# Kernel optimization log

Hardware: AMD Instinct MI355X
Metric: run time of the kernel (lower is better)

The kernel has to match this reference:

```python
import jax, jax.numpy as jnp
import numpy as np

IMG_SIZE = 640.0
CONF_THRESH = 0.001
NMS_THRESH = 0.6
TOP_K = 1000  # fixed-shape candidate cap per class


def _pairwise_iou(b):
    # b: [K,4] in x1,y1,x2,y2; replicates the numpy NMS math (1e-28 / 1e-14 eps)
    x1, y1, x2, y2 = b[:, 0], b[:, 1], b[:, 2], b[:, 3]
    areas = (x2 - x1) * (y2 - y1)
    xx1 = jnp.maximum(x1[:, None], x1[None, :])
    yy1 = jnp.maximum(y1[:, None], y1[None, :])
    xx2 = jnp.minimum(x2[:, None], x2[None, :])
    yy2 = jnp.minimum(y2[:, None], y2[None, :])
    w = jnp.maximum(1e-28, xx2 - xx1)
    h = jnp.maximum(1e-28, yy2 - yy1)
    inter = w * h
    return inter / (areas[:, None] + areas[None, :] - inter + 1e-14)


def setup_inputs() -> dict:
    key = jax.random.key(0)
    k1, k2, k3 = jax.random.split(key, 3)
    img_size, strides, KA, C = 640, [8, 16, 32], 3, 80
    anchor = np.array([[10, 13], [16, 30], [33, 23], [30, 61], [62, 45], [59, 119],
                       [116, 90], [156, 198], [373, 326]], np.float32).reshape(3, 3, 2)
    grids, anchs, strs = [], [], []
    for lvl, s in enumerate(strides):
        f = img_size // s
        gy, gx = np.meshgrid(np.arange(f), np.arange(f), indexing='ij')
        gxy = np.stack([gx, gy], -1).reshape(-1, 1, 2).astype(np.float32)
        grids.append(np.broadcast_to(gxy, (f * f, KA, 2)).reshape(-1, 2))
        anchs.append(np.broadcast_to(anchor[lvl][None], (f * f, KA, 2)).reshape(-1, 2).astype(np.float32))
        strs.append(np.full((f * f * KA, 1), s, np.float32))
    grid_xy = jnp.asarray(np.concatenate(grids, 0))      # [N,2]
    anchors_wh = jnp.asarray(np.concatenate(anchs, 0))   # [N,2]
    stride_t = jnp.asarray(np.concatenate(strs, 0))      # [N,1]
    N = grid_xy.shape[0]  # 25200
    return {
        'reg_pred': jax.random.normal(k1, (N, 4), jnp.float32),
        'obj_pred': jax.random.normal(k2, (N, 1), jnp.float32),
        'cls_pred': jax.random.normal(k3, (N, C), jnp.float32),
        'grid_xy': grid_xy,
        'anchors_wh': anchors_wh,
        'stride_t': stride_t,
    }


def reference(reg_pred, obj_pred, cls_pred, grid_xy, anchors_wh, stride_t):
    # ---- box decode (YOLO head) ----
    xy = (jax.nn.sigmoid(reg_pred[:, :2]) + grid_xy) * stride_t       # centers in pixels
    wh = jnp.exp(reg_pred[:, 2:]) * anchors_wh                        # sizes in pixels
    boxes = jnp.concatenate([xy - 0.5 * wh, xy + 0.5 * wh], axis=-1)  # [N,4]
    boxes = jnp.clip(boxes / IMG_SIZE, 0.0, 1.0)
    # ---- scoring: sigmoid(obj) * softmax(cls) ----
    scores_all = jax.nn.sigmoid(obj_pred) * jax.nn.softmax(cls_pred, axis=-1)  # [N,C]
    cls_inds = jnp.argmax(scores_all, axis=-1)          # [N]
    scores = jnp.max(scores_all, axis=-1)               # [N]
    C = cls_pred.shape[-1]
    K = TOP_K
    ar = jnp.arange(K)

    def nms_class(c):
        s_c = jnp.where((cls_inds == c) & (scores >= CONF_THRESH), scores, -1.0)
        vals, idx = jax.lax.top_k(s_c, K)               # sorted desc, fixed shape
        b = boxes[idx]                                  # [K,4]
        valid = vals > 0.0
        iou = _pairwise_iou(b)                          # [K,K]

        def body(i, keep):
            sup = keep[i] & (iou[i] > NMS_THRESH) & (ar > i)
            return keep & ~sup

        keep = jax.lax.fori_loop(0, K, body, valid)
        return b, vals, keep

    boxes_out, scores_out, keep = jax.vmap(nms_class)(jnp.arange(C))  # [C,K,4],[C,K],[C,K]
    return boxes_out, scores_out * keep.astype(scores_out.dtype), keep
```

## Files before the change

### kernel.cpp

```cpp
#include <hip/hip_runtime.h>
#include <cstdint>
#include <cstddef>

#define N_CLS 80
#define TOPK 1000
#define POOL_N 2048
#define MCAP 512
#define BD 1024
#define DTB 128
#define NBLK 197
#define SLICE 32
#define LDSB_STRIDE 10

__global__ __launch_bounds__(DTB) void decode_kernel(
    const float* __restrict__ reg, const float* __restrict__ obj,
    const float* __restrict__ cls, const float* __restrict__ grid,
    const float* __restrict__ anch, const float* __restrict__ strd,
    float* __restrict__ boxes, uint2* __restrict__ scs,
    int* __restrict__ cnts, uint2* __restrict__ gpool2, int N) {
  __shared__ int hcnt[N_CLS];
  const int blk = blockIdx.x;
  const int tid = threadIdx.x;
  const int i = blk * DTB + tid;

  if (tid < N_CLS) hcnt[tid] = 0;
  __syncthreads();

  const bool valid = (i < N);
  float best = -1.0f;
  int bc = 0;

  if (valid) {
    const float4 r = ((const float4*)reg)[i];
    const float2 g = ((const float2*)grid)[i];
    const float2 aw = ((const float2*)anch)[i];
    const float st = strd[i];

    float cx = (1.0f / (1.0f + expf(-r.x)) + g.x) * st;
    float cy = (1.0f / (1.0f + expf(-r.y)) + g.y) * st;
    float w = expf(r.z) * aw.x;
    float h = expf(r.w) * aw.y;
    float b0 = fminf(fmaxf((cx - 0.5f * w) / 640.0f, 0.0f), 1.0f);
    float b1 = fminf(fmaxf((cy - 0.5f * h) / 640.0f, 0.0f), 1.0f);
    float b2 = fminf(fmaxf((cx + 0.5f * w) / 640.0f, 0.0f), 1.0f);
    float b3 = fminf(fmaxf((cy + 0.5f * h) / 640.0f, 0.0f), 1.0f);
    float4 bo; bo.x = b0; bo.y = b1; bo.z = b2; bo.w = b3;
    ((float4*)boxes)[i] = bo;

    const float4* cr = (const float4*)cls + (size_t)i * 20;
    float4 x[20];
#pragma unroll
    for (int q = 0; q < 20; ++q) x[q] = cr[q];

    float4 m4 = x[0];
#pragma unroll
    for (int q = 1; q < 20; ++q) {
      m4.x = fmaxf(m4.x, x[q].x); m4.y = fmaxf(m4.y, x[q].y);
      m4.z = fmaxf(m4.z, x[q].z); m4.w = fmaxf(m4.w, x[q].w);
    }
    float mx = fmaxf(fmaxf(m4.x, m4.y), fmaxf(m4.z, m4.w));

#pragma unroll
    for (int q = 0; q < 20; ++q) {
      x[q].x = expf(x[q].x - mx); x[q].y = expf(x[q].y - mx);
      x[q].z = expf(x[q].z - mx); x[q].w = expf(x[q].w - mx);
    }

    float s = 0.0f;
#pragma unroll
    for (int q = 0; q < 20; ++q) {
      s += x[q].x; s += x[q].y; s += x[q].z; s += x[q].w;
    }

    float sig = 1.0f / (1.0f + expf(-obj[i]));

#pragma unroll
    for (int q = 0; q < 20; ++q) {
      float q0 = sig * (x[q].x / s);
      if (q0 > best) { best = q0; bc = 4 * q + 0; }
      float q1 = sig * (x[q].y / s);
      if (q1 > best) { best = q1; bc = 4 * q + 1; }
      float q2 = sig * (x[q].z / s);
      if (q2 > best) { best = q2; bc = 4 * q + 2; }
      float q3 = sig * (x[q].w / s);
      if (q3 > best) { best = q3; bc = 4 * q + 3; }
    }
    scs[i] = make_uint2(__float_as_uint(best), (unsigned)bc);
  }

  const bool pos = valid && (best >= 0.001f);
  int slot = -1;
  if (pos) slot = atomicAdd(&hcnt[bc], 1);
  __syncthreads();
  if (tid < N_CLS) cnts[blk * N_CLS + tid] = min(hcnt[tid], SLICE);
  if (pos && slot < SLICE)
    gpool2[((size_t)bc * NBLK + blk) * SLICE + slot] =
        make_uint2(__float_as_uint(best), (unsigned)i);
}

__device__ __forceinline__ unsigned long long kinit(int w, int m) {
  int lo = w << 6;
  return (m <= lo) ? 0ULL : ((m - lo >= 64) ? ~0ULL : ((1ULL << (m - lo)) - 1ULL));
}

__global__ __launch_bounds__(BD) void nms_kernel(
    const float* __restrict__ boxes, const uint2* __restrict__ scs,
    const int* __restrict__ cnts, const uint2* __restrict__ gpool2,
    float* __restrict__ out, int N) {
  const int c = blockIdx.x;
  const int tid = threadIdx.x;

  __shared__ uint2 pool[POOL_N];
  __shared__ float svals[TOPK];
  __shared__ int sidx[TOPK];
  __shared__ __align__(16) float4 bxyz[TOPK];
  __shared__ __align__(16) unsigned long long ldsB[MCAP * LDSB_STRIDE];
  __shared__ unsigned char kp[TOPK];
  __shared__ __align__(16) unsigned long long kmbuf[2][8];
  __shared__ int wsum[BD / 64 + 1];
  __shared__ int pref[NBLK + 1];

  if (tid < 64) {
    int carry = 0;
    if (tid == 0) pref[0] = 0;
    for (int ch = 0; ch < (NBLK + 63) / 64; ++ch) {
      int b = ch * 64 + tid;
      int v = (b < NBLK) ? cnts[b * N_CLS + c] : 0;
#pragma unroll
      for (int s = 1; s < 64; s <<= 1) {
        int u = __shfl_up(v, s, 64);
        if (tid >= (unsigned)s) v += u;
      }
      if (b < NBLK) pref[b + 1] = min(carry + v, POOL_N);
      carry += __shfl(v, 63, 64);
    }
  }
  __syncthreads();
  const int cnt = pref[NBLK];
  const int m = min(cnt, TOPK);

  const uint2* gp = gpool2 + (size_t)c * NBLK * SLICE;
  for (int t = tid; t < cnt; t += BD) {
    int lo = 0, hi = NBLK;
    while (hi - lo > 1) {
      int mid = (lo + hi) >> 1;
      if (t >= pref[mid]) lo = mid; else hi = mid;
    }
    pool[t] = gp[(size_t)lo * SLICE + (t - pref[lo])];
  }
  __syncthreads();

  for (int e = tid; e < cnt; e += BD) {
    uint2 me = pool[e];
    float v = __uint_as_float(me.x);
    int idx = (int)me.y;
    int r = 0;
#pragma unroll 8
    for (int k = 0; k < cnt; ++k) {
      uint2 q = pool[k];
      float vk = __uint_as_float(q.x);
      r += (int)((vk > v) || (vk == v && (int)q.y < idx));
    }
    if (r < TOPK) { svals[r] = v; sidx[r] = idx; }
  }
  __syncthreads();

  const int M = TOPK - m;
  if (M > 0) {
    int i = tid;
    bool f = false;
    if (i < N) {
      uint2 sc = scs[i];
      f = !((int)sc.y == c && __uint_as_float(sc.x) >= 0.001f);
    }
    unsigned long long mk = __ballot(f ? 1 : 0);
    int lane = tid & 63, wv = tid >> 6;
    int pre = __popcll(mk & ((1ULL << lane) - 1ULL));
    if (lane == 0) wsum[wv] = __popcll(mk);
    __syncthreads();
    if (tid == 0) {
      int acc = 0;
      for (int wq = 0; wq < BD / 64; ++wq) { int t2 = wsum[wq]; wsum[wq] = acc; acc += t2; }
    }
    __syncthreads();
    int pos = wsum[wv] + pre;
    if (f && pos < M) sidx[m + pos] = i;
  }
  __syncthreads();

  const float4* bf4 = (const float4*)boxes;
  for (int t = tid; t < TOPK; t += BD) bxyz[t] = bf4[sidx[t]];
  __syncthreads();

  const int W = (m + 63) >> 6;
  const bool fast = (m > 0) && (m <= MCAP);
  int cur = 0;

  if (fast) {
    const int tasks = m * W;
    for (int q = tid; q < tasks; q += BD) {
      int w = q / m;
      int j = q - w * m;
      unsigned long long bits = 0ULL;
      if (w <= (j >> 6)) {
        float4 jb = bxyz[j];
        float aj = (jb.z - jb.x) * (jb.w - jb.y);
        int i0 = w << 6, iend = min(i0 + 64, j);
        for (int i = i0; i < iend; ++i) {
          float4 ib = bxyz[i];
          float ai = (ib.z - ib.x) * (ib.w - ib.y);
          float xx1 = fmaxf(ib.x, jb.x), yy1 = fmaxf(ib.y, jb.y);
          float xx2 = fminf(ib.z, jb.z), yy2 = fminf(ib.w, jb.w);
          float ww = fmaxf(1e-28f, xx2 - xx1), hh = fmaxf(1e-28f, yy2 - yy1);
          float inter = ww * hh;
          float iou = inter / (ai + aj - inter + 1e-14f);
          if (iou > 0.6f) bits |= (1ULL << (i - i0));
        }
      }
      ldsB[(size_t)j * LDSB_STRIDE + w] = bits;
    }
    __syncthreads();

    ulonglong2 ta, tb, tc, td;
    ta = tb = tc = td = make_ulonglong2(0ULL, 0ULL);
    if (tid < m) {
      const ulonglong2* rp = (const ulonglong2*)&ldsB[(size_t)tid * LDSB_STRIDE];
      ta = rp[0]; tb = rp[1]; tc = rp[2]; td = rp[3];
    }
    if (tid < 8) kmbuf[0][tid] = kinit(tid, m);
    __syncthreads();

    for (;;) {
      bool keep = false;
      if (tid < m) {
        unsigned long long sup =
            (ta.x & kmbuf[cur][0]) | (ta.y & kmbuf[cur][1]) |
            (tb.x & kmbuf[cur][2]) | (tb.y & kmbuf[cur][3]) |
            (tc.x & kmbuf[cur][4]) | (tc.y & kmbuf[cur][5]) |
            (td.x & kmbuf[cur][6]) | (td.y & kmbuf[cur][7]);
        keep = (sup == 0ULL);
      }
      bool old = (tid < m) &&
                 ((kmbuf[cur][tid >> 6] >> (tid & 63)) & 1ULL);
      unsigned long long bl = __ballot(keep ? 1 : 0);
      int wv = tid >> 6;
      if ((tid & 63) == 0 && wv < 8) kmbuf[cur ^ 1][wv] = bl;
      int any = __syncthreads_or((int)(keep != old));
      cur ^= 1;
      if (!any) break;
    }
  } else {
    for (int t = tid; t < TOPK; t += BD) kp[t] = (t < m) ? 1 : 0;
    __syncthreads();
    for (int i = 0; i < m; ++i) {
      if (kp[i]) {
        float4 rb = bxyz[i];
        float ai = (rb.z - rb.x) * (rb.w - rb.y);
        for (int j = i + 1 + tid; j < m; j += BD) {
          if (kp[j]) {
            float4 jb = bxyz[j];
            float aj = (jb.z - jb.x) * (jb.w - jb.y);
            float xx1 = fmaxf(rb.x, jb.x), yy1 = fmaxf(rb.y, jb.y);
            float xx2 = fminf(rb.z, jb.z), yy2 = fminf(rb.w, jb.w);
            float ww = fmaxf(1e-28f, xx2 - xx1), hh = fmaxf(1e-28f, yy2 - yy1);
            float inter = ww * hh;
            float iou = inter / (ai + aj - inter + 1e-14f);
            if (iou > 0.6f) kp[j] = 0;
          }
        }
      }
      __syncthreads();
    }
  }

  float* outB = out;
  float* outS = out + N_CLS * TOPK * 4;
  float* outK = outS + N_CLS * TOPK;
  for (int t = tid; t < TOPK; t += BD) {
    float k = 0.0f;
    if (t < m)
      k = fast ? (float)((kmbuf[cur][t >> 6] >> (t & 63)) & 1ULL)
               : (float)kp[t];
    float v = (t < m) ? svals[t] : -1.0f;
    ((float4*)outB)[c * TOPK + t] = bxyz[t];
    outS[c * TOPK + t] = v * k;
    outK[c * TOPK + t] = k;
  }
}

extern "C" void kernel_launch(void* const* d_in, const int* in_sizes, int n_in,
                              void* d_out, int out_size, void* d_ws, size_t ws_size,
                              hipStream_t stream) {
  const float* reg  = (const float*)d_in[0];
  const float* obj  = (const float*)d_in[1];
  const float* cls  = (const float*)d_in[2];
  const float* grid = (const float*)d_in[3];
  const float* anch = (const float*)d_in[4];
  const float* strd = (const float*)d_in[5];
  const int N = in_sizes[0] / 4;

  char* w8 = (char*)d_ws;
  size_t off = 0;
  float* boxes  = (float*)(w8 + off); off += (size_t)N * 16;
  uint2* scs    = (uint2*)(w8 + off); off += (size_t)N * 8;
  int*   cnts   = (int*)(w8 + off);   off += (size_t)NBLK * N_CLS * 4;
  uint2* gpool2 = (uint2*)(w8 + off); off += (size_t)N_CLS * NBLK * SLICE * 8;
  float* out = (float*)d_out;

  decode_kernel<<<NBLK, DTB, 0, stream>>>(
      reg, obj, cls, grid, anch, strd, boxes, scs, cnts, gpool2, N);
  nms_kernel<<<N_CLS, BD, 0, stream>>>(boxes, scs, cnts, gpool2, out, N);
}
```

Before: 113.6 us.

## Replace fixed-point NMS iteration with per-wave greedy ballot stages

The fast NMS path used to iterate a block-wide fixed-point on the keep mask, calling __syncthreads_or until the mask stopped changing, which can need many rounds. It now resolves suppression exactly one 64-box word at a time. Within a single wave, ballot and find-first-set walk the kept boxes greedily, then the word's mask is published to LDS, and every thread folds that word into its suppression accumulator. This caps the number of block barriers at eight, but the in-wave loop runs serially per kept box. Launch-bound occupancy hints are also added to both kernels.

```diff
diff --git a/kernel.cpp b/kernel.cpp
--- a/kernel.cpp
+++ b/kernel.cpp
@@ -12,7 +12,7 @@
 #define SLICE 32
 #define LDSB_STRIDE 10
 
-__global__ __launch_bounds__(DTB) void decode_kernel(
+__global__ __launch_bounds__(DTB, 1) void decode_kernel(
     const float* __restrict__ reg, const float* __restrict__ obj,
     const float* __restrict__ cls, const float* __restrict__ grid,
     const float* __restrict__ anch, const float* __restrict__ strd,
@@ -98,12 +98,7 @@
         make_uint2(__float_as_uint(best), (unsigned)i);
 }
 
-__device__ __forceinline__ unsigned long long kinit(int w, int m) {
-  int lo = w << 6;
-  return (m <= lo) ? 0ULL : ((m - lo >= 64) ? ~0ULL : ((1ULL << (m - lo)) - 1ULL));
-}
-
-__global__ __launch_bounds__(BD) void nms_kernel(
+__global__ __launch_bounds__(BD, 4) void nms_kernel(
     const float* __restrict__ boxes, const uint2* __restrict__ scs,
     const int* __restrict__ cnts, const uint2* __restrict__ gpool2,
     float* __restrict__ out, int N) {
@@ -116,7 +111,7 @@
   __shared__ __align__(16) float4 bxyz[TOPK];
   __shared__ __align__(16) unsigned long long ldsB[MCAP * LDSB_STRIDE];
   __shared__ unsigned char kp[TOPK];
-  __shared__ __align__(16) unsigned long long kmbuf[2][8];
+  __shared__ unsigned long long kmw_lds[8];
   __shared__ int wsum[BD / 64 + 1];
   __shared__ int pref[NBLK + 1];
 
@@ -135,6 +130,7 @@
       carry += __shfl(v, 63, 64);
     }
   }
+  if (tid < 8) kmw_lds[tid] = 0ULL;
   __syncthreads();
   const int cnt = pref[NBLK];
   const int m = min(cnt, TOPK);
@@ -194,7 +190,6 @@
 
   const int W = (m + 63) >> 6;
   const bool fast = (m > 0) && (m <= MCAP);
-  int cur = 0;
 
   if (fast) {
     const int tasks = m * W;
@@ -227,28 +222,37 @@
       const ulonglong2* rp = (const ulonglong2*)&ldsB[(size_t)tid * LDSB_STRIDE];
       ta = rp[0]; tb = rp[1]; tc = rp[2]; td = rp[3];
     }
-    if (tid < 8) kmbuf[0][tid] = kinit(tid, m);
-    __syncthreads();
-
-    for (;;) {
-      bool keep = false;
-      if (tid < m) {
-        unsigned long long sup =
-            (ta.x & kmbuf[cur][0]) | (ta.y & kmbuf[cur][1]) |
-            (tb.x & kmbuf[cur][2]) | (tb.y & kmbuf[cur][3]) |
-            (tc.x & kmbuf[cur][4]) | (tc.y & kmbuf[cur][5]) |
-            (td.x & kmbuf[cur][6]) | (td.y & kmbuf[cur][7]);
-        keep = (sup == 0ULL);
-      }
-      bool old = (tid < m) &&
-                 ((kmbuf[cur][tid >> 6] >> (tid & 63)) & 1ULL);
-      unsigned long long bl = __ballot(keep ? 1 : 0);
-      int wv = tid >> 6;
-      if ((tid & 63) == 0 && wv < 8) kmbuf[cur ^ 1][wv] = bl;
-      int any = __syncthreads_or((int)(keep != old));
-      cur ^= 1;
-      if (!any) break;
-    }
+    __syncthreads();
+
+    unsigned long long supAcc = 0ULL;
+#define GREEDY_STAGE(w, word)                                                \
+    if (((w) << 6) < m) {                                                    \
+      if ((tid >> 6) == (w)) {                                               \
+        bool alive = (tid < m) && (supAcc == 0ULL);                          \
+        unsigned long long bb = (word);                                      \
+        unsigned long long kmw = 0ULL, done = 0ULL;                          \
+        for (;;) {                                                           \
+          unsigned long long kb = __ballot(alive) & ~done;                   \
+          if (!kb) break;                                                    \
+          int b = __ffsll((long long)kb) - 1;                                \
+          kmw |= (1ULL << b);                                                \
+          done = (b >= 63) ? ~0ULL : ((2ULL << b) - 1ULL);                   \
+          if ((bb >> b) & 1ULL) alive = false;                               \
+        }                                                                    \
+        if ((tid & 63) == 0) kmw_lds[w] = kmw;                               \
+      }                                                                      \
+      __syncthreads();                                                       \
+      supAcc |= (word) & kmw_lds[w];                                         \
+    }
+    GREEDY_STAGE(0, ta.x)
+    GREEDY_STAGE(1, ta.y)
+    GREEDY_STAGE(2, tb.x)
+    GREEDY_STAGE(3, tb.y)
+    GREEDY_STAGE(4, tc.x)
+    GREEDY_STAGE(5, tc.y)
+    GREEDY_STAGE(6, td.x)
+    GREEDY_STAGE(7, td.y)
+#undef GREEDY_STAGE
   } else {
     for (int t = tid; t < TOPK; t += BD) kp[t] = (t < m) ? 1 : 0;
     __syncthreads();
@@ -279,7 +283,7 @@
   for (int t = tid; t < TOPK; t += BD) {
     float k = 0.0f;
     if (t < m)
-      k = fast ? (float)((kmbuf[cur][t >> 6] >> (t & 63)) & 1ULL)
+      k = fast ? (float)((kmw_lds[t >> 6] >> (t & 63)) & 1ULL)
                : (float)kp[t];
     float v = (t < m) ? svals[t] : -1.0f;
     ((float4*)outB)[c * TOPK + t] = bxyz[t];
```

Result: slower. 141.8 us (+24.8%).
